# Kernel tuning notes

Hardware: AMD Instinct MI355X
Metric: run time of the kernel (lower is better)

Reference implementation:

```python
import jax, jax.numpy as jnp
import numpy as np

B, C, W = 16, 256, 64


def qlinear(x, Wm, b):
    # x: (b, Cin, 4); Wm: (4, Cout, Cin); b: (4, Cout)
    # Separate linear per quaternion component, then Hamilton-like combine.
    comps = jnp.einsum('bic,coi->boc', x, Wm) + b.T[None]  # (b, Cout, 4)
    r, xc, yc, zc = comps[..., 0], comps[..., 1], comps[..., 2], comps[..., 3]
    return jnp.stack([
        r + xc + yc + zc,
        xc - r - zc + yc,
        yc + zc - r - xc,
        zc - yc + xc - r,
    ], axis=-1)  # (b, Cout, 4)


def setup_inputs() -> dict:
    key = jax.random.key(0)
    k0, k1, k2, k3, k4 = jax.random.split(key, 5)
    return {
        'x': jax.random.normal(k0, (B, C, W, W, 4), dtype=jnp.float32),
        'comp_w': jax.random.normal(k1, (4, 1, C), dtype=jnp.float32) * (1.0 / np.sqrt(C)),
        'comp_b': jax.random.normal(k2, (4, 1), dtype=jnp.float32) * 0.01,
        'exc_w': jax.random.normal(k3, (4, C, 1), dtype=jnp.float32),
        'exc_b': jax.random.normal(k4, (4, C), dtype=jnp.float32) * 0.01,
    }


def reference(x, comp_w, comp_b, exc_w, exc_b):
    # Global max pool over spatial dims, per quaternion component: (b, C, 4)
    pooled = jnp.max(x, axis=(2, 3))
    u = qlinear(pooled, comp_w, comp_b)          # (b, 1, 4)
    u = qlinear(u, exc_w, exc_b)                 # (b, C, 4)
    # Broadcast per-channel, per-component scale over spatial dims
    return x * u[:, :, None, None, :]
```

## Files before the change

kernel.cpp:

```cpp
#include <hip/hip_runtime.h>

#define B 16
#define C 256
#define SPATIAL 4096

typedef float vf4 __attribute__((ext_vector_type(4)));

__global__ __launch_bounds__(256) void pool_kernel(const float4* __restrict__ x4,
                                                   float4* __restrict__ pooled4) {
    const int bc = blockIdx.x;
    const float4* p = x4 + (size_t)bc * SPATIAL;
    const int tid = threadIdx.x;

    float4 m = p[tid];
    #pragma unroll
    for (int s = tid + 256; s < SPATIAL; s += 256) {
        float4 v = p[s];
        m.x = fmaxf(m.x, v.x);
        m.y = fmaxf(m.y, v.y);
        m.z = fmaxf(m.z, v.z);
        m.w = fmaxf(m.w, v.w);
    }

    #pragma unroll
    for (int off = 32; off > 0; off >>= 1) {
        m.x = fmaxf(m.x, __shfl_down(m.x, off));
        m.y = fmaxf(m.y, __shfl_down(m.y, off));
        m.z = fmaxf(m.z, __shfl_down(m.z, off));
        m.w = fmaxf(m.w, __shfl_down(m.w, off));
    }

    __shared__ float4 lm[4];
    const int lane = tid & 63, wid = tid >> 6;
    if (lane == 0) lm[wid] = m;
    __syncthreads();
    if (tid == 0) {
        float4 r = lm[0];
        #pragma unroll
        for (int w = 1; w < 4; ++w) {
            r.x = fmaxf(r.x, lm[w].x);
            r.y = fmaxf(r.y, lm[w].y);
            r.z = fmaxf(r.z, lm[w].z);
            r.w = fmaxf(r.w, lm[w].w);
        }
        pooled4[bc] = r;
    }
}

__global__ __launch_bounds__(256) void scale_mul_kernel(const float4* __restrict__ x4,
                                                        const float4* __restrict__ pooled4,
                                                        const float* __restrict__ comp_w,
                                                        const float* __restrict__ comp_b,
                                                        const float* __restrict__ exc_w,
                                                        const float* __restrict__ exc_b,
                                                        float4* __restrict__ out4) {
    const int bc  = (B * C - 1) - blockIdx.x;
    const int b   = bc >> 8;
    const int c   = bc & (C - 1);
    const int tid = threadIdx.x;

    float4 p = pooled4[b * C + tid];
    float4 prod;
    prod.x = p.x * comp_w[0 * C + tid];
    prod.y = p.y * comp_w[1 * C + tid];
    prod.z = p.z * comp_w[2 * C + tid];
    prod.w = p.w * comp_w[3 * C + tid];

    #pragma unroll
    for (int off = 32; off > 0; off >>= 1) {
        prod.x += __shfl_down(prod.x, off);
        prod.y += __shfl_down(prod.y, off);
        prod.z += __shfl_down(prod.z, off);
        prod.w += __shfl_down(prod.w, off);
    }

    __shared__ float4 lsum[4];
    const int lane = tid & 63, wid = tid >> 6;
    if (lane == 0) lsum[wid] = prod;
    __syncthreads();

    const float r  = lsum[0].x + lsum[1].x + lsum[2].x + lsum[3].x + comp_b[0];
    const float xc = lsum[0].y + lsum[1].y + lsum[2].y + lsum[3].y + comp_b[1];
    const float yc = lsum[0].z + lsum[1].z + lsum[2].z + lsum[3].z + comp_b[2];
    const float zc = lsum[0].w + lsum[1].w + lsum[2].w + lsum[3].w + comp_b[3];

    const float u0 = r + xc + yc + zc;
    const float u1 = xc - r - zc + yc;
    const float u2 = yc + zc - r - xc;
    const float u3 = zc - yc + xc - r;

    const float c0 = u0 * exc_w[0 * C + c] + exc_b[0 * C + c];
    const float c1 = u1 * exc_w[1 * C + c] + exc_b[1 * C + c];
    const float c2 = u2 * exc_w[2 * C + c] + exc_b[2 * C + c];
    const float c3 = u3 * exc_w[3 * C + c] + exc_b[3 * C + c];

    vf4 s;
    s.x = c0 + c1 + c2 + c3;
    s.y = c1 - c0 - c3 + c2;
    s.z = c2 + c3 - c0 - c1;
    s.w = c3 - c2 + c1 - c0;

    const vf4* xp = (const vf4*)(x4 + (size_t)bc * SPATIAL);
    vf4*       op = (vf4*)(out4 + (size_t)bc * SPATIAL);
    #pragma unroll 4
    for (int i = tid; i < SPATIAL; i += 256) {
        vf4 v = xp[i];
        v *= s;
        __builtin_nontemporal_store(v, op + i);
    }
}

extern "C" void kernel_launch(void* const* d_in, const int* in_sizes, int n_in,
                              void* d_out, int out_size, void* d_ws, size_t ws_size,
                              hipStream_t stream) {
    const float4* x4     = (const float4*)d_in[0];
    const float*  comp_w = (const float*)d_in[1];
    const float*  comp_b = (const float*)d_in[2];
    const float*  exc_w  = (const float*)d_in[3];
    const float*  exc_b  = (const float*)d_in[4];
    float4* out4 = (float4*)d_out;

    float4* pooled4 = (float4*)d_ws;

    pool_kernel<<<B * C, 256, 0, stream>>>(x4, pooled4);
    scale_mul_kernel<<<B * C, 256, 0, stream>>>(x4, pooled4, comp_w, comp_b,
                                                exc_w, exc_b, out4);
}
```

Measured before the change: 483.4 us.

## Split scale computation into own kernel and use one wave per channel in pooling

Pooling now gives each wavefront one (b,c) channel, which removes the LDS reduction and block barrier. The per-batch scale computation moves into a small 16-block kernel, so the 4096 multiply blocks no longer each redo the 256-wide dot-product reduction. The multiply kernel just loads one precomputed float4 scale and streams, with a deeper unroll. This adds a third kernel launch and an extra dependency step, and each pooling wave now reads 64KB on its own.

```diff
diff --git a/kernel.cpp b/kernel.cpp
--- a/kernel.cpp
+++ b/kernel.cpp
@@ -2,20 +2,22 @@
 
 #define B 16
 #define C 256
+#define BC (B * C)
 #define SPATIAL 4096
 
 typedef float vf4 __attribute__((ext_vector_type(4)));
 
 __global__ __launch_bounds__(256) void pool_kernel(const float4* __restrict__ x4,
                                                    float4* __restrict__ pooled4) {
-    const int bc = blockIdx.x;
+    const int wid  = threadIdx.x >> 6;
+    const int lane = threadIdx.x & 63;
+    const int bc   = (blockIdx.x << 2) + wid;
     const float4* p = x4 + (size_t)bc * SPATIAL;
-    const int tid = threadIdx.x;
 
-    float4 m = p[tid];
-    #pragma unroll
-    for (int s = tid + 256; s < SPATIAL; s += 256) {
-        float4 v = p[s];
+    float4 m = p[lane];
+    #pragma unroll 7
+    for (int k = 1; k < 64; ++k) {
+        float4 v = p[lane + (k << 6)];
         m.x = fmaxf(m.x, v.x);
         m.y = fmaxf(m.y, v.y);
         m.z = fmaxf(m.z, v.z);
@@ -29,34 +31,16 @@
         m.z = fmaxf(m.z, __shfl_down(m.z, off));
         m.w = fmaxf(m.w, __shfl_down(m.w, off));
     }
-
-    __shared__ float4 lm[4];
-    const int lane = tid & 63, wid = tid >> 6;
-    if (lane == 0) lm[wid] = m;
-    __syncthreads();
-    if (tid == 0) {
-        float4 r = lm[0];
-        #pragma unroll
-        for (int w = 1; w < 4; ++w) {
-            r.x = fmaxf(r.x, lm[w].x);
-            r.y = fmaxf(r.y, lm[w].y);
-            r.z = fmaxf(r.z, lm[w].z);
-            r.w = fmaxf(r.w, lm[w].w);
-        }
-        pooled4[bc] = r;
-    }
+    if (lane == 0) pooled4[bc] = m;
 }
 
-__global__ __launch_bounds__(256) void scale_mul_kernel(const float4* __restrict__ x4,
-                                                        const float4* __restrict__ pooled4,
-                                                        const float* __restrict__ comp_w,
-                                                        const float* __restrict__ comp_b,
-                                                        const float* __restrict__ exc_w,
-                                                        const float* __restrict__ exc_b,
-                                                        float4* __restrict__ out4) {
-    const int bc  = (B * C - 1) - blockIdx.x;
-    const int b   = bc >> 8;
-    const int c   = bc & (C - 1);
+__global__ __launch_bounds__(256) void scales_kernel(const float4* __restrict__ pooled4,
+                                                     const float* __restrict__ comp_w,
+                                                     const float* __restrict__ comp_b,
+                                                     const float* __restrict__ exc_w,
+                                                     const float* __restrict__ exc_b,
+                                                     float4* __restrict__ s4) {
+    const int b   = blockIdx.x;
     const int tid = threadIdx.x;
 
     float4 p = pooled4[b * C + tid];
@@ -89,21 +73,34 @@
     const float u2 = yc + zc - r - xc;
     const float u3 = zc - yc + xc - r;
 
+    const int c = tid;
     const float c0 = u0 * exc_w[0 * C + c] + exc_b[0 * C + c];
     const float c1 = u1 * exc_w[1 * C + c] + exc_b[1 * C + c];
     const float c2 = u2 * exc_w[2 * C + c] + exc_b[2 * C + c];
     const float c3 = u3 * exc_w[3 * C + c] + exc_b[3 * C + c];
 
-    vf4 s;
+    float4 s;
     s.x = c0 + c1 + c2 + c3;
     s.y = c1 - c0 - c3 + c2;
     s.z = c2 + c3 - c0 - c1;
     s.w = c3 - c2 + c1 - c0;
+    s4[b * C + c] = s;
+}
+
+__global__ __launch_bounds__(256) void mul_kernel(const float4* __restrict__ x4,
+                                                  const float4* __restrict__ s4,
+                                                  float4* __restrict__ out4) {
+    const int bc = (BC - 1) - blockIdx.x;
+
+    const float4 sf = s4[bc];
+    vf4 s;
+    s.x = sf.x; s.y = sf.y; s.z = sf.z; s.w = sf.w;
 
     const vf4* xp = (const vf4*)(x4 + (size_t)bc * SPATIAL);
     vf4*       op = (vf4*)(out4 + (size_t)bc * SPATIAL);
-    #pragma unroll 4
-    for (int i = tid; i < SPATIAL; i += 256) {
+
+    #pragma unroll 8
+    for (int i = threadIdx.x; i < SPATIAL; i += 256) {
         vf4 v = xp[i];
         v *= s;
         __builtin_nontemporal_store(v, op + i);
@@ -121,8 +118,9 @@
     float4* out4 = (float4*)d_out;
 
     float4* pooled4 = (float4*)d_ws;
+    float4* s4      = pooled4 + BC;
 
-    pool_kernel<<<B * C, 256, 0, stream>>>(x4, pooled4);
-    scale_mul_kernel<<<B * C, 256, 0, stream>>>(x4, pooled4, comp_w, comp_b,
-                                                exc_w, exc_b, out4);
+    pool_kernel<<<BC / 4, 256, 0, stream>>>(x4, pooled4);
+    scales_kernel<<<B, 256, 0, stream>>>(pooled4, comp_w, comp_b, exc_w, exc_b, s4);
+    mul_kernel<<<BC, 256, 0, stream>>>(x4, s4, out4);
 }
```

New measurement: 484.6 us. No clear change (+0.3%).
